# Kernel optimization log

Measured on AMD Instinct MI355X. Metric: run time of the kernel, lower is better.

## Reference

```python
import jax, jax.numpy as jnp
import numpy as np

N = 500000   # number of points
C = 64       # in_channels == out_channels
L = 4        # n_layers


def setup_inputs() -> dict:
    key = jax.random.key(0)
    ks = jax.random.split(key, 7)
    s = np.float32(1.0 / np.sqrt(C))  # keep activations O(1) across layers
    return {
        "features": jax.random.normal(ks[0], (N, C), jnp.float32),
        "points": jax.random.normal(ks[1], (N, 3), jnp.float32),
        "nuv": jax.random.normal(ks[2], (N, 3, 3), jnp.float32),
        "W0": jax.random.normal(ks[3], (L, C, C), jnp.float32) * s,  # linear_transform
        "b0": jnp.zeros((L, C), jnp.float32),
        "W1": jax.random.normal(ks[4], (L, C, C), jnp.float32) * s,  # linear_block[0]
        "b1": jnp.zeros((L, C), jnp.float32),
        "W2": jax.random.normal(ks[5], (L, C, C), jnp.float32) * s,  # linear_block[2]
        "b2": jnp.zeros((L, C), jnp.float32),
    }


def reference(features, points, nuv, W0, b0, W1, b1, W2, b2):
    # Faithful to the torch source: inside each DMaSIFConvBlock the dmasif_conv
    # output is overwritten by linear_transform(features), so the effective math
    # per block is: x = Linear2(relu(Linear1(Linear0(x)))).
    # points / nuv / ranges do not influence the output.
    del points, nuv

    def step(x, params):
        w0, c0, w1, c1, w2, c2 = params
        h = x @ w0 + c0                      # linear_transform
        h = jax.nn.relu(h @ w1 + c1)          # linear_block: Linear + ReLU
        h = h @ w2 + c2                      # linear_block: Linear
        return h, None

    out, _ = jax.lax.scan(step, features, (W0, b0, W1, b1, W2, b2))
    return out
```

## Files before the change

### kernel.cpp

```cpp
#include <hip/hip_runtime.h>
#include <stdint.h>

#define CH 64
#define NPTS 500000
#define NTILE (NPTS / 32)
#define NSTEP 12
#define BLK 256

typedef float floatx16 __attribute__((ext_vector_type(16)));
typedef __bf16 bf16x8 __attribute__((ext_vector_type(8)));

__device__ __forceinline__ unsigned pk(float odd, float even) {
    return __builtin_amdgcn_perm(__float_as_uint(odd), __float_as_uint(even), 0x07060302u);
}
__device__ __forceinline__ float hif(float x) {
    return __uint_as_float(__float_as_uint(x) & 0xffff0000u);
}

struct U16 { unsigned a, b, c, d; };
__device__ __forceinline__ bf16x8 asb4(unsigned x0, unsigned x1, unsigned x2, unsigned x3) {
    U16 t{x0, x1, x2, x3};
    return __builtin_bit_cast(bf16x8, t);
}
__device__ __forceinline__ bf16x8 asbu4(uint4 v) {
    return __builtin_bit_cast(bf16x8, v);
}

__global__ void prep_weights(const float* __restrict__ W0,
                             const float* __restrict__ W1,
                             const float* __restrict__ W2,
                             uint4* __restrict__ wsA) {
    const int g  = blockIdx.x * blockDim.x + threadIdx.x;
    const int mp = g & 31;
    const int h  = (g >> 5) & 1;
    const int q  = (g >> 6) & 3;
    const int mt = (g >> 8) & 1;
    const int pl = (g >> 9) & 1;
    const int s  = g >> 10;
    const float* Wb = (s % 3 == 0) ? W0 : ((s % 3 == 1) ? W1 : W2);
    const float* Ws = Wb + (s / 3) * CH * CH;
    const int m   = mt * 32 + mp;
    const int col = (m & ~12) | ((m & 4) << 1) | ((m & 8) >> 1);
    unsigned o[4];
    #pragma unroll
    for (int d = 0; d < 4; ++d) {
        float e = Ws[(16 * q + 8 * h + 2 * d) * CH + col];
        float v = Ws[(16 * q + 8 * h + 2 * d + 1) * CH + col];
        if (pl) { e = e - hif(e); v = v - hif(v); }
        o[d] = pk(v, e);
    }
    wsA[g] = make_uint4(o[0], o[1], o[2], o[3]);
}

__global__ __launch_bounds__(BLK) void mlp12_mfma(
    const float* __restrict__ feat,
    const uint4* __restrict__ wsA,
    const float* __restrict__ b0,
    const float* __restrict__ b1,
    const float* __restrict__ b2,
    float* __restrict__ out)
{
    const int lane = threadIdx.x & 63;
    const int wid  = blockIdx.x * (BLK / 64) + (threadIdx.x >> 6);
    if (wid >= NTILE) return;
    const int n = lane & 31;
    const int h = lane >> 5;
    const size_t row = (size_t)(wid * 32 + n) * CH;

    float4 fa[4], fb[4];
    {
        const float* frow = feat + row + 8 * h;
        #pragma unroll
        for (int q = 0; q < 4; ++q) {
            fa[q] = *(const float4*)(frow + 16 * q);
            fb[q] = *(const float4*)(frow + 16 * q + 4);
        }
    }

    unsigned Bhi[4][4], Blo[4][4];
    floatx16 acc0, acc1;

    #pragma unroll
    for (int s = 0; s < NSTEP; ++s) {
        uint4 A[2][2][4];
        #pragma unroll
        for (int pl = 0; pl < 2; ++pl)
            #pragma unroll
            for (int mt = 0; mt < 2; ++mt)
                #pragma unroll
                for (int q = 0; q < 4; ++q)
                    A[pl][mt][q] = wsA[(((((s * 2 + pl) * 2 + mt) * 4 + q)) << 6) + lane];

        const float* bs = ((s % 3 == 0) ? b0 : (s % 3 == 1) ? b1 : b2) + (s / 3) * CH;
        float4 bv[2][4];
        #pragma unroll
        for (int mt = 0; mt < 2; ++mt)
            #pragma unroll
            for (int rq = 0; rq < 4; ++rq)
                bv[mt][rq] = *(const float4*)(bs + 32 * mt + 16 * (rq >> 1) + 8 * h + 4 * (rq & 1));

        if (s == 0) {
            #pragma unroll
            for (int q = 0; q < 4; ++q) {
                float e0 = fa[q].x, o0 = fa[q].y, e1 = fa[q].z, o1 = fa[q].w;
                float e2 = fb[q].x, o2 = fb[q].y, e3 = fb[q].z, o3 = fb[q].w;
                Bhi[q][0] = pk(o0, e0); Bhi[q][1] = pk(o1, e1);
                Bhi[q][2] = pk(o2, e2); Bhi[q][3] = pk(o3, e3);
                Blo[q][0] = pk(o0 - hif(o0), e0 - hif(e0));
                Blo[q][1] = pk(o1 - hif(o1), e1 - hif(e1));
                Blo[q][2] = pk(o2 - hif(o2), e2 - hif(e2));
                Blo[q][3] = pk(o3 - hif(o3), e3 - hif(e3));
            }
        } else {
            const bool relu = (s % 3 == 2);
            #pragma unroll
            for (int q = 0; q < 4; ++q) {
                const int rr = q & 1;
                #pragma unroll
                for (int d = 0; d < 4; ++d) {
                    float e, o;
                    if (q < 2) { e = acc0[8 * rr + 2 * d]; o = acc0[8 * rr + 2 * d + 1]; }
                    else       { e = acc1[8 * rr + 2 * d]; o = acc1[8 * rr + 2 * d + 1]; }
                    if (relu) { e = fmaxf(e, 0.f); o = fmaxf(o, 0.f); }
                    Bhi[q][d] = pk(o, e);
                    Blo[q][d] = pk(o - hif(o), e - hif(e));
                }
            }
        }

        #pragma unroll
        for (int rq = 0; rq < 4; ++rq) {
            acc0[4 * rq + 0] = bv[0][rq].x; acc0[4 * rq + 1] = bv[0][rq].y;
            acc0[4 * rq + 2] = bv[0][rq].z; acc0[4 * rq + 3] = bv[0][rq].w;
            acc1[4 * rq + 0] = bv[1][rq].x; acc1[4 * rq + 1] = bv[1][rq].y;
            acc1[4 * rq + 2] = bv[1][rq].z; acc1[4 * rq + 3] = bv[1][rq].w;
        }

        #pragma unroll
        for (int q = 0; q < 4; ++q) {
            bf16x8 bh = asb4(Bhi[q][0], Bhi[q][1], Bhi[q][2], Bhi[q][3]);
            bf16x8 bl = asb4(Blo[q][0], Blo[q][1], Blo[q][2], Blo[q][3]);
            acc0 = __builtin_amdgcn_mfma_f32_32x32x16_bf16(asbu4(A[0][0][q]), bh, acc0, 0, 0, 0);
            acc1 = __builtin_amdgcn_mfma_f32_32x32x16_bf16(asbu4(A[0][1][q]), bh, acc1, 0, 0, 0);
            acc0 = __builtin_amdgcn_mfma_f32_32x32x16_bf16(asbu4(A[1][0][q]), bh, acc0, 0, 0, 0);
            acc1 = __builtin_amdgcn_mfma_f32_32x32x16_bf16(asbu4(A[1][1][q]), bh, acc1, 0, 0, 0);
            acc0 = __builtin_amdgcn_mfma_f32_32x32x16_bf16(asbu4(A[0][0][q]), bl, acc0, 0, 0, 0);
            acc1 = __builtin_amdgcn_mfma_f32_32x32x16_bf16(asbu4(A[0][1][q]), bl, acc1, 0, 0, 0);
        }
    }

    float* orow = out + row;
    #pragma unroll
    for (int rq = 0; rq < 4; ++rq) {
        float4 v0, v1;
        v0.x = acc0[4 * rq + 0]; v0.y = acc0[4 * rq + 1];
        v0.z = acc0[4 * rq + 2]; v0.w = acc0[4 * rq + 3];
        v1.x = acc1[4 * rq + 0]; v1.y = acc1[4 * rq + 1];
        v1.z = acc1[4 * rq + 2]; v1.w = acc1[4 * rq + 3];
        const int off = 16 * (rq >> 1) + 8 * h + 4 * (rq & 1);
        *(float4*)(orow + off)      = v0;
        *(float4*)(orow + 32 + off) = v1;
    }
}

extern "C" void kernel_launch(void* const* d_in, const int* in_sizes, int n_in,
                              void* d_out, int out_size, void* d_ws, size_t ws_size,
                              hipStream_t stream) {
    const float* feat = (const float*)d_in[0];
    const float* W0 = (const float*)d_in[3];
    const float* b0 = (const float*)d_in[4];
    const float* W1 = (const float*)d_in[5];
    const float* b1 = (const float*)d_in[6];
    const float* W2 = (const float*)d_in[7];
    const float* b2 = (const float*)d_in[8];
    float* out = (float*)d_out;
    uint4* wsA = (uint4*)d_ws;

    prep_weights<<<48, 256, 0, stream>>>(W0, W1, W2, wsA);

    const int grid = (NTILE + (BLK / 64) - 1) / (BLK / 64);
    mlp12_mfma<<<grid, BLK, 0, stream>>>(feat, wsA, b0, b1, b2, out);
}
```

Measured before the change: 368.9 us.

## Stage per-step weight fragments in LDS via async global_load_lds double buffering

Per-step MFMA weight fragments are no longer loaded straight from global memory into registers by every wave. Each block now cooperatively streams them into a double-buffered LDS area with global_load_lds, prefetching step s+1 while step s computes. A block barrier at each step keeps the buffers safe, and the out-of-range waves are clamped rather than returning early so they still reach the barriers. A minimum-blocks hint is added to launch bounds. The aim is to cut redundant global and L2 weight traffic and the register pressure of holding all A fragments. The cost is 12 block barriers per tile and 32KB of LDS per block.

```diff
diff --git a/kernel.cpp b/kernel.cpp
--- a/kernel.cpp
+++ b/kernel.cpp
@@ -6,6 +6,7 @@
 #define NTILE (NPTS / 32)
 #define NSTEP 12
 #define BLK 256
+#define WPB (BLK / 64)
 
 typedef float floatx16 __attribute__((ext_vector_type(16)));
 typedef __bf16 bf16x8 __attribute__((ext_vector_type(8)));
@@ -24,6 +25,12 @@
 }
 __device__ __forceinline__ bf16x8 asbu4(uint4 v) {
     return __builtin_bit_cast(bf16x8, v);
+}
+
+typedef __attribute__((address_space(3))) void lds_void;
+typedef const __attribute__((address_space(1))) void gm_void;
+__device__ __forceinline__ void gload_lds16(const void* g, void* l) {
+    __builtin_amdgcn_global_load_lds((gm_void*)g, (lds_void*)l, 16, 0, 0);
 }
 
 __global__ void prep_weights(const float* __restrict__ W0,
@@ -52,7 +59,7 @@
     wsA[g] = make_uint4(o[0], o[1], o[2], o[3]);
 }
 
-__global__ __launch_bounds__(BLK) void mlp12_mfma(
+__global__ __launch_bounds__(BLK, 4) void mlp12_mfma(
     const float* __restrict__ feat,
     const uint4* __restrict__ wsA,
     const float* __restrict__ b0,
@@ -60,9 +67,13 @@
     const float* __restrict__ b2,
     float* __restrict__ out)
 {
-    const int lane = threadIdx.x & 63;
-    const int wid  = blockIdx.x * (BLK / 64) + (threadIdx.x >> 6);
-    if (wid >= NTILE) return;
+    __shared__ uint4 sA[2][1024];
+
+    const int tid  = threadIdx.x;
+    const int lane = tid & 63;
+    const int wv   = tid >> 6;
+    int wid = blockIdx.x * WPB + wv;
+    if (wid > NTILE - 1) wid = NTILE - 1;
     const int n = lane & 31;
     const int h = lane >> 5;
     const size_t row = (size_t)(wid * 32 + n) * CH;
@@ -77,27 +88,35 @@
         }
     }
 
+    {
+        const char* g = (const char*)wsA;
+        #pragma unroll
+        for (int c = 0; c < 4; ++c)
+            gload_lds16(g + (wv * 4 + c) * 1024 + lane * 16,
+                        (char*)&sA[0][0] + (wv * 4 + c) * 1024);
+    }
+    __syncthreads();
+
     unsigned Bhi[4][4], Blo[4][4];
     floatx16 acc0, acc1;
 
     #pragma unroll
     for (int s = 0; s < NSTEP; ++s) {
-        uint4 A[2][2][4];
-        #pragma unroll
-        for (int pl = 0; pl < 2; ++pl)
-            #pragma unroll
-            for (int mt = 0; mt < 2; ++mt)
-                #pragma unroll
-                for (int q = 0; q < 4; ++q)
-                    A[pl][mt][q] = wsA[(((((s * 2 + pl) * 2 + mt) * 4 + q)) << 6) + lane];
-
-        const float* bs = ((s % 3 == 0) ? b0 : (s % 3 == 1) ? b1 : b2) + (s / 3) * CH;
-        float4 bv[2][4];
-        #pragma unroll
-        for (int mt = 0; mt < 2; ++mt)
-            #pragma unroll
-            for (int rq = 0; rq < 4; ++rq)
-                bv[mt][rq] = *(const float4*)(bs + 32 * mt + 16 * (rq >> 1) + 8 * h + 4 * (rq & 1));
+        const int b = s & 1;
+
+        if (s + 1 < NSTEP) {
+            const char* g = (const char*)wsA + (size_t)(s + 1) * 16384;
+            #pragma unroll
+            for (int c = 0; c < 4; ++c)
+                gload_lds16(g + (wv * 4 + c) * 1024 + lane * 16,
+                            (char*)&sA[1 - b][0] + (wv * 4 + c) * 1024);
+        }
+
+        const uint4* base = &sA[b][0];
+
+        uint4 Acur[4], Anx[4];
+        #pragma unroll
+        for (int t = 0; t < 4; ++t) Acur[t] = base[(t * 4 + 0) * 64 + lane];
 
         if (s == 0) {
             #pragma unroll
@@ -128,25 +147,39 @@
             }
         }
 
-        #pragma unroll
-        for (int rq = 0; rq < 4; ++rq) {
-            acc0[4 * rq + 0] = bv[0][rq].x; acc0[4 * rq + 1] = bv[0][rq].y;
-            acc0[4 * rq + 2] = bv[0][rq].z; acc0[4 * rq + 3] = bv[0][rq].w;
-            acc1[4 * rq + 0] = bv[1][rq].x; acc1[4 * rq + 1] = bv[1][rq].y;
-            acc1[4 * rq + 2] = bv[1][rq].z; acc1[4 * rq + 3] = bv[1][rq].w;
+        {
+            const float* bs = ((s % 3 == 0) ? b0 : (s % 3 == 1) ? b1 : b2) + (s / 3) * CH;
+            #pragma unroll
+            for (int rq = 0; rq < 4; ++rq) {
+                const int off = 16 * (rq >> 1) + 8 * h + 4 * (rq & 1);
+                float4 v0 = *(const float4*)(bs + off);
+                float4 v1 = *(const float4*)(bs + 32 + off);
+                acc0[4 * rq + 0] = v0.x; acc0[4 * rq + 1] = v0.y;
+                acc0[4 * rq + 2] = v0.z; acc0[4 * rq + 3] = v0.w;
+                acc1[4 * rq + 0] = v1.x; acc1[4 * rq + 1] = v1.y;
+                acc1[4 * rq + 2] = v1.z; acc1[4 * rq + 3] = v1.w;
+            }
         }
 
         #pragma unroll
         for (int q = 0; q < 4; ++q) {
+            if (q < 3) {
+                #pragma unroll
+                for (int t = 0; t < 4; ++t) Anx[t] = base[(t * 4 + q + 1) * 64 + lane];
+            }
             bf16x8 bh = asb4(Bhi[q][0], Bhi[q][1], Bhi[q][2], Bhi[q][3]);
             bf16x8 bl = asb4(Blo[q][0], Blo[q][1], Blo[q][2], Blo[q][3]);
-            acc0 = __builtin_amdgcn_mfma_f32_32x32x16_bf16(asbu4(A[0][0][q]), bh, acc0, 0, 0, 0);
-            acc1 = __builtin_amdgcn_mfma_f32_32x32x16_bf16(asbu4(A[0][1][q]), bh, acc1, 0, 0, 0);
-            acc0 = __builtin_amdgcn_mfma_f32_32x32x16_bf16(asbu4(A[1][0][q]), bh, acc0, 0, 0, 0);
-            acc1 = __builtin_amdgcn_mfma_f32_32x32x16_bf16(asbu4(A[1][1][q]), bh, acc1, 0, 0, 0);
-            acc0 = __builtin_amdgcn_mfma_f32_32x32x16_bf16(asbu4(A[0][0][q]), bl, acc0, 0, 0, 0);
-            acc1 = __builtin_amdgcn_mfma_f32_32x32x16_bf16(asbu4(A[0][1][q]), bl, acc1, 0, 0, 0);
-        }
+            acc0 = __builtin_amdgcn_mfma_f32_32x32x16_bf16(asbu4(Acur[0]), bh, acc0, 0, 0, 0);
+            acc1 = __builtin_amdgcn_mfma_f32_32x32x16_bf16(asbu4(Acur[1]), bh, acc1, 0, 0, 0);
+            acc0 = __builtin_amdgcn_mfma_f32_32x32x16_bf16(asbu4(Acur[2]), bh, acc0, 0, 0, 0);
+            acc1 = __builtin_amdgcn_mfma_f32_32x32x16_bf16(asbu4(Acur[3]), bh, acc1, 0, 0, 0);
+            acc0 = __builtin_amdgcn_mfma_f32_32x32x16_bf16(asbu4(Acur[0]), bl, acc0, 0, 0, 0);
+            acc1 = __builtin_amdgcn_mfma_f32_32x32x16_bf16(asbu4(Acur[1]), bl, acc1, 0, 0, 0);
+            #pragma unroll
+            for (int t = 0; t < 4; ++t) Acur[t] = Anx[t];
+        }
+
+        __syncthreads();
     }
 
     float* orow = out + row;
@@ -178,6 +211,6 @@
 
     prep_weights<<<48, 256, 0, stream>>>(W0, W1, W2, wsA);
 
-    const int grid = (NTILE + (BLK / 64) - 1) / (BLK / 64);
+    const int grid = (NTILE + WPB - 1) / WPB;
     mlp12_mfma<<<grid, BLK, 0, stream>>>(feat, wsA, b0, b1, b2, out);
 }
```

Measured after the change: 335.8 us. 1.1x faster.

## Double-buffer weight fragments, stage biases in LDS, interleave split-bf16 packing with MFMA

Applied to the files above, without the earlier changes.

Prefetches the next layer's weight fragments into a second register buffer while the current layer's MFMAs run. All twelve bias vectors are staged once per block in shared memory. Packing of the hi/lo bf16 operands is moved into the per-q MFMA loop using double-buffered accumulators, so conversion can overlap matrix work. Out-of-range waves are clamped to the last tile instead of returning early, so the block-wide barrier stays safe. The costs are higher register pressure from the extra weight and accumulator buffers, which launch_bounds(BLK,2) tries to contain, and redundant duplicate writes of the last tile by clamped waves.

```diff
diff --git a/kernel.cpp b/kernel.cpp
--- a/kernel.cpp
+++ b/kernel.cpp
@@ -6,8 +6,10 @@
 #define NTILE (NPTS / 32)
 #define NSTEP 12
 #define BLK 256
+#define WPB (BLK / 64)
 
 typedef float floatx16 __attribute__((ext_vector_type(16)));
+typedef float f32x8 __attribute__((ext_vector_type(8)));
 typedef __bf16 bf16x8 __attribute__((ext_vector_type(8)));
 
 __device__ __forceinline__ unsigned pk(float odd, float even) {
@@ -52,7 +54,7 @@
     wsA[g] = make_uint4(o[0], o[1], o[2], o[3]);
 }
 
-__global__ __launch_bounds__(BLK) void mlp12_mfma(
+__global__ __launch_bounds__(BLK, 2) void mlp12_mfma(
     const float* __restrict__ feat,
     const uint4* __restrict__ wsA,
     const float* __restrict__ b0,
@@ -60,9 +62,12 @@
     const float* __restrict__ b2,
     float* __restrict__ out)
 {
-    const int lane = threadIdx.x & 63;
-    const int wid  = blockIdx.x * (BLK / 64) + (threadIdx.x >> 6);
-    if (wid >= NTILE) return;
+    __shared__ __align__(16) float sBias[NSTEP * CH];
+
+    const int tid  = threadIdx.x;
+    const int lane = tid & 63;
+    int wid = blockIdx.x * WPB + (tid >> 6);
+    if (wid > NTILE - 1) wid = NTILE - 1;
     const int n = lane & 31;
     const int h = lane >> 5;
     const size_t row = (size_t)(wid * 32 + n) * CH;
@@ -77,75 +82,80 @@
         }
     }
 
-    unsigned Bhi[4][4], Blo[4][4];
-    floatx16 acc0, acc1;
+    uint4 Abuf[2][16];
+    #pragma unroll
+    for (int g = 0; g < 16; ++g) Abuf[0][g] = wsA[g * 64 + lane];
+
+    #pragma unroll
+    for (int t = tid; t < NSTEP * CH; t += BLK) {
+        const int s = t >> 6;
+        const float* bs = ((s % 3 == 0) ? b0 : (s % 3 == 1) ? b1 : b2) + (s / 3) * CH;
+        sBias[t] = bs[t & 63];
+    }
+    __syncthreads();
+
+    floatx16 acc[2][2];
 
     #pragma unroll
     for (int s = 0; s < NSTEP; ++s) {
-        uint4 A[2][2][4];
+        const int p   = s & 1;
+        const int dst = s & 1;
+        const int src = dst ^ 1;
+
+        if (s + 1 < NSTEP) {
+            const uint4* wn = wsA + (size_t)(s + 1) * 1024;
+            #pragma unroll
+            for (int g = 0; g < 16; ++g) Abuf[p ^ 1][g] = wn[g * 64 + lane];
+        }
+
+        {
+            const float* bb = &sBias[s * CH];
+            f32x8 c0a = *(const f32x8*)(bb + 8 * h);
+            f32x8 c0b = *(const f32x8*)(bb + 16 + 8 * h);
+            f32x8 c1a = *(const f32x8*)(bb + 32 + 8 * h);
+            f32x8 c1b = *(const f32x8*)(bb + 48 + 8 * h);
+            #pragma unroll
+            for (int j = 0; j < 8; ++j) {
+                acc[dst][0][j]     = c0a[j];
+                acc[dst][0][8 + j] = c0b[j];
+                acc[dst][1][j]     = c1a[j];
+                acc[dst][1][8 + j] = c1b[j];
+            }
+        }
+
+        const bool relu = (s % 3 == 2);
+
         #pragma unroll
-        for (int pl = 0; pl < 2; ++pl)
-            #pragma unroll
-            for (int mt = 0; mt < 2; ++mt)
-                #pragma unroll
-                for (int q = 0; q < 4; ++q)
-                    A[pl][mt][q] = wsA[(((((s * 2 + pl) * 2 + mt) * 4 + q)) << 6) + lane];
-
-        const float* bs = ((s % 3 == 0) ? b0 : (s % 3 == 1) ? b1 : b2) + (s / 3) * CH;
-        float4 bv[2][4];
-        #pragma unroll
-        for (int mt = 0; mt < 2; ++mt)
-            #pragma unroll
-            for (int rq = 0; rq < 4; ++rq)
-                bv[mt][rq] = *(const float4*)(bs + 32 * mt + 16 * (rq >> 1) + 8 * h + 4 * (rq & 1));
-
-        if (s == 0) {
-            #pragma unroll
-            for (int q = 0; q < 4; ++q) {
+        for (int q = 0; q < 4; ++q) {
+            unsigned bhq[4], blq[4];
+            if (s == 0) {
                 float e0 = fa[q].x, o0 = fa[q].y, e1 = fa[q].z, o1 = fa[q].w;
                 float e2 = fb[q].x, o2 = fb[q].y, e3 = fb[q].z, o3 = fb[q].w;
-                Bhi[q][0] = pk(o0, e0); Bhi[q][1] = pk(o1, e1);
-                Bhi[q][2] = pk(o2, e2); Bhi[q][3] = pk(o3, e3);
-                Blo[q][0] = pk(o0 - hif(o0), e0 - hif(e0));
-                Blo[q][1] = pk(o1 - hif(o1), e1 - hif(e1));
-                Blo[q][2] = pk(o2 - hif(o2), e2 - hif(e2));
-                Blo[q][3] = pk(o3 - hif(o3), e3 - hif(e3));
-            }
-        } else {
-            const bool relu = (s % 3 == 2);
-            #pragma unroll
-            for (int q = 0; q < 4; ++q) {
+                bhq[0] = pk(o0, e0); bhq[1] = pk(o1, e1);
+                bhq[2] = pk(o2, e2); bhq[3] = pk(o3, e3);
+                blq[0] = pk(o0 - hif(o0), e0 - hif(e0));
+                blq[1] = pk(o1 - hif(o1), e1 - hif(e1));
+                blq[2] = pk(o2 - hif(o2), e2 - hif(e2));
+                blq[3] = pk(o3 - hif(o3), e3 - hif(e3));
+            } else {
                 const int rr = q & 1;
                 #pragma unroll
                 for (int d = 0; d < 4; ++d) {
-                    float e, o;
-                    if (q < 2) { e = acc0[8 * rr + 2 * d]; o = acc0[8 * rr + 2 * d + 1]; }
-                    else       { e = acc1[8 * rr + 2 * d]; o = acc1[8 * rr + 2 * d + 1]; }
+                    float e = acc[src][q >> 1][8 * rr + 2 * d];
+                    float o = acc[src][q >> 1][8 * rr + 2 * d + 1];
                     if (relu) { e = fmaxf(e, 0.f); o = fmaxf(o, 0.f); }
-                    Bhi[q][d] = pk(o, e);
-                    Blo[q][d] = pk(o - hif(o), e - hif(e));
+                    bhq[d] = pk(o, e);
+                    blq[d] = pk(o - hif(o), e - hif(e));
                 }
             }
-        }
-
-        #pragma unroll
-        for (int rq = 0; rq < 4; ++rq) {
-            acc0[4 * rq + 0] = bv[0][rq].x; acc0[4 * rq + 1] = bv[0][rq].y;
-            acc0[4 * rq + 2] = bv[0][rq].z; acc0[4 * rq + 3] = bv[0][rq].w;
-            acc1[4 * rq + 0] = bv[1][rq].x; acc1[4 * rq + 1] = bv[1][rq].y;
-            acc1[4 * rq + 2] = bv[1][rq].z; acc1[4 * rq + 3] = bv[1][rq].w;
-        }
-
-        #pragma unroll
-        for (int q = 0; q < 4; ++q) {
-            bf16x8 bh = asb4(Bhi[q][0], Bhi[q][1], Bhi[q][2], Bhi[q][3]);
-            bf16x8 bl = asb4(Blo[q][0], Blo[q][1], Blo[q][2], Blo[q][3]);
-            acc0 = __builtin_amdgcn_mfma_f32_32x32x16_bf16(asbu4(A[0][0][q]), bh, acc0, 0, 0, 0);
-            acc1 = __builtin_amdgcn_mfma_f32_32x32x16_bf16(asbu4(A[0][1][q]), bh, acc1, 0, 0, 0);
-            acc0 = __builtin_amdgcn_mfma_f32_32x32x16_bf16(asbu4(A[1][0][q]), bh, acc0, 0, 0, 0);
-            acc1 = __builtin_amdgcn_mfma_f32_32x32x16_bf16(asbu4(A[1][1][q]), bh, acc1, 0, 0, 0);
-            acc0 = __builtin_amdgcn_mfma_f32_32x32x16_bf16(asbu4(A[0][0][q]), bl, acc0, 0, 0, 0);
-            acc1 = __builtin_amdgcn_mfma_f32_32x32x16_bf16(asbu4(A[0][1][q]), bl, acc1, 0, 0, 0);
+            bf16x8 bh = asb4(bhq[0], bhq[1], bhq[2], bhq[3]);
+            bf16x8 bl = asb4(blq[0], blq[1], blq[2], blq[3]);
+            acc[dst][0] = __builtin_amdgcn_mfma_f32_32x32x16_bf16(asbu4(Abuf[p][q]),      bh, acc[dst][0], 0, 0, 0);
+            acc[dst][1] = __builtin_amdgcn_mfma_f32_32x32x16_bf16(asbu4(Abuf[p][4 + q]),  bh, acc[dst][1], 0, 0, 0);
+            acc[dst][0] = __builtin_amdgcn_mfma_f32_32x32x16_bf16(asbu4(Abuf[p][8 + q]),  bh, acc[dst][0], 0, 0, 0);
+            acc[dst][1] = __builtin_amdgcn_mfma_f32_32x32x16_bf16(asbu4(Abuf[p][12 + q]), bh, acc[dst][1], 0, 0, 0);
+            acc[dst][0] = __builtin_amdgcn_mfma_f32_32x32x16_bf16(asbu4(Abuf[p][q]),      bl, acc[dst][0], 0, 0, 0);
+            acc[dst][1] = __builtin_amdgcn_mfma_f32_32x32x16_bf16(asbu4(Abuf[p][4 + q]),  bl, acc[dst][1], 0, 0, 0);
         }
     }
 
@@ -153,10 +163,10 @@
     #pragma unroll
     for (int rq = 0; rq < 4; ++rq) {
         float4 v0, v1;
-        v0.x = acc0[4 * rq + 0]; v0.y = acc0[4 * rq + 1];
-        v0.z = acc0[4 * rq + 2]; v0.w = acc0[4 * rq + 3];
-        v1.x = acc1[4 * rq + 0]; v1.y = acc1[4 * rq + 1];
-        v1.z = acc1[4 * rq + 2]; v1.w = acc1[4 * rq + 3];
+        v0.x = acc[1][0][4 * rq + 0]; v0.y = acc[1][0][4 * rq + 1];
+        v0.z = acc[1][0][4 * rq + 2]; v0.w = acc[1][0][4 * rq + 3];
+        v1.x = acc[1][1][4 * rq + 0]; v1.y = acc[1][1][4 * rq + 1];
+        v1.z = acc[1][1][4 * rq + 2]; v1.w = acc[1][1][4 * rq + 3];
         const int off = 16 * (rq >> 1) + 8 * h + 4 * (rq & 1);
         *(float4*)(orow + off)      = v0;
         *(float4*)(orow + 32 + off) = v1;
@@ -178,6 +188,6 @@
 
     prep_weights<<<48, 256, 0, stream>>>(W0, W1, W2, wsA);
 
-    const int grid = (NTILE + (BLK / 64) - 1) / (BLK / 64);
+    const int grid = (NTILE + WPB - 1) / WPB;
     mlp12_mfma<<<grid, BLK, 0, stream>>>(feat, wsA, b0, b1, b2, out);
 }
```

New measurement: 353.0 us. 1.05x faster.
